# Optimization experiments

Measured on AMD Instinct MI355X. Metric: run time of the kernel, lower is better.

The kernel has to match this reference:

```python
import jax, jax.numpy as jnp
import numpy as np

B, N, T, D, H, E = 2, 1024, 8, 128, 4, 8192
DH = D // H
NEG_SLOPE = 0.2  # GATv2Conv default negative_slope


def _ln(x, g, b):
    m = jnp.mean(x, -1, keepdims=True)
    v = jnp.mean((x - m) ** 2, -1, keepdims=True)
    return (x - m) * jax.lax.rsqrt(v + 1e-5) * g + b


def _forward(x, edge_index, gat_wl, gat_wr, gat_att, gat_b, in_w, in_b, out_w, out_b,
             ffn_w1, ffn_b1, ffn_w2, ffn_b2, fus_w, fus_b,
             lns_g, lns_b, lnt1_g, lnt1_b, lnt2_g, lnt2_b, lnf_g, lnf_b):
    # ---- spatial branch: GATv2, vectorized over (B, T) instead of python loops ----
    loops = jnp.arange(N)
    src = jnp.concatenate([edge_index[0], loops])  # j: message source (PyG adds self loops)
    dst = jnp.concatenate([edge_index[1], loops])  # i: aggregation target
    xl = jnp.einsum('bntd,de->bnte', x, gat_wl).reshape(B, N, T, H, D)
    xr = jnp.einsum('bntd,de->bnte', x, gat_wr).reshape(B, N, T, H, D)
    ml = xl[:, src]                                  # [B,Et,T,H,D]
    mr = xr[:, dst]
    e = jax.nn.leaky_relu(ml + mr, NEG_SLOPE)
    logits = jnp.einsum('bethd,hd->beth', e, gat_att)
    logits = jnp.moveaxis(logits, 1, 0)              # [Et,B,T,H]
    mx = jax.ops.segment_max(logits, dst, num_segments=N)
    p = jnp.exp(logits - mx[dst])                    # stable edge softmax per dst node
    ssum = jax.ops.segment_sum(p, dst, num_segments=N)
    alpha = p / ssum[dst]                            # [Et,B,T,H]
    msg = alpha[..., None] * jnp.moveaxis(ml, 1, 0)
    agg = jax.ops.segment_sum(msg, dst, num_segments=N)  # [N,B,T,H,D]
    x_sp = jnp.moveaxis(agg.mean(3), 0, 1) + gat_b   # concat=False -> head mean; [B,N,T,D]
    x_sp = _ln(x_sp, lns_g, lns_b)

    # ---- temporal branch: MHA + FFN, vectorized over all B*N nodes ----
    xt = x.reshape(B * N, T, D)
    qkv = xt @ in_w + in_b
    q, k, v = jnp.split(qkv, 3, axis=-1)
    q = q.reshape(B * N, T, H, DH)
    k = k.reshape(B * N, T, H, DH)
    v = v.reshape(B * N, T, H, DH)
    scores = jnp.einsum('bthd,bshd->bhts', q, k) / np.float32(np.sqrt(DH))
    attn = jax.nn.softmax(scores, -1)
    o = jnp.einsum('bhts,bshd->bthd', attn, v).reshape(B * N, T, D)
    o = o @ out_w + out_b
    x1 = _ln(xt + o, lnt1_g, lnt1_b)
    ffn = jax.nn.gelu(x1 @ ffn_w1 + ffn_b1, approximate=False) @ ffn_w2 + ffn_b2
    x_tp = _ln(x1 + ffn, lnt2_g, lnt2_b).reshape(B, N, T, D)

    # ---- gated fusion with residual ----
    g = jax.nn.sigmoid(jnp.concatenate([x_sp, x_tp], -1) @ fus_w + fus_b)
    return _ln(g * x_sp + (1.0 - g) * x_tp + x, lnf_g, lnf_b)


def setup_inputs() -> dict:
    key = jax.random.key(0)
    ks = jax.random.split(key, 12)
    s = 0.05
    f = jnp.float32
    return {
        'x': jax.random.normal(ks[0], (B, N, T, D), f),
        'edge_index': jax.random.randint(ks[1], (2, E), 0, N),
        'gat_wl': jax.random.normal(ks[2], (D, H * D), f) * s,
        'gat_wr': jax.random.normal(ks[3], (D, H * D), f) * s,
        'gat_att': jax.random.normal(ks[4], (H, D), f) * s,
        'gat_b': jnp.zeros((D,), f),
        'in_w': jax.random.normal(ks[5], (D, 3 * D), f) * s,
        'in_b': jnp.zeros((3 * D,), f),
        'out_w': jax.random.normal(ks[6], (D, D), f) * s,
        'out_b': jnp.zeros((D,), f),
        'ffn_w1': jax.random.normal(ks[7], (D, 4 * D), f) * s,
        'ffn_b1': jnp.zeros((4 * D,), f),
        'ffn_w2': jax.random.normal(ks[8], (4 * D, D), f) * s,
        'ffn_b2': jnp.zeros((D,), f),
        'fus_w': jax.random.normal(ks[9], (2 * D, D), f) * s,
        'fus_b': jnp.zeros((D,), f),
        'lns_g': jnp.ones((D,), f), 'lns_b': jnp.zeros((D,), f),
        'lnt1_g': jnp.ones((D,), f), 'lnt1_b': jnp.zeros((D,), f),
        'lnt2_g': jnp.ones((D,), f), 'lnt2_b': jnp.zeros((D,), f),
        'lnf_g': jnp.ones((D,), f), 'lnf_b': jnp.zeros((D,), f),
    }


def reference(x, edge_index, gat_wl, gat_wr, gat_att, gat_b, in_w, in_b, out_w, out_b,
              ffn_w1, ffn_b1, ffn_w2, ffn_b2, fus_w, fus_b,
              lns_g, lns_b, lnt1_g, lnt1_b, lnt2_g, lnt2_b, lnf_g, lnf_b):
    return _forward(x, edge_index, gat_wl, gat_wr, gat_att, gat_b, in_w, in_b, out_w, out_b,
                    ffn_w1, ffn_b1, ffn_w2, ffn_b2, fus_w, fus_b,
                    lns_g, lns_b, lnt1_g, lnt1_b, lnt2_g, lnt2_b, lnf_g, lnf_b)
```

## Files before the change

kernel.cpp:

```cpp
#include <hip/hip_runtime.h>
#include <math.h>

#define B_ 2
#define N_ 1024
#define T_ 8
#define D_ 128
#define H_ 4
#define E_ 8192
#define EN_ 9216
#define M_ 16384

typedef unsigned short u16;
using bf16x8 = __attribute__((ext_vector_type(8))) short;
using f32x4  = __attribute__((ext_vector_type(4))) float;

__device__ __forceinline__ float bf2f(unsigned int u) {
  return __uint_as_float(u << 16);
}
__device__ __forceinline__ u16 f2bf(float f) {
  unsigned int x = __float_as_uint(f);
  x += 0x7fffu + ((x >> 16) & 1u);
  return (u16)(x >> 16);
}
__device__ __forceinline__ void load8f(const u16* p, float* f) {
  uint4 u = *(const uint4*)p;
  f[0]=bf2f(u.x & 0xffffu); f[1]=bf2f(u.x >> 16);
  f[2]=bf2f(u.y & 0xffffu); f[3]=bf2f(u.y >> 16);
  f[4]=bf2f(u.z & 0xffffu); f[5]=bf2f(u.z >> 16);
  f[6]=bf2f(u.w & 0xffffu); f[7]=bf2f(u.w >> 16);
}
__device__ __forceinline__ void unpack8(uint4 u, float* f) {
  f[0]=bf2f(u.x & 0xffffu); f[1]=bf2f(u.x >> 16);
  f[2]=bf2f(u.y & 0xffffu); f[3]=bf2f(u.y >> 16);
  f[4]=bf2f(u.z & 0xffffu); f[5]=bf2f(u.z >> 16);
  f[6]=bf2f(u.w & 0xffffu); f[7]=bf2f(u.w >> 16);
}
__device__ __forceinline__ void gl2lds(const u16* g, u16* l) {
  __builtin_amdgcn_global_load_lds(
      (const __attribute__((address_space(1))) unsigned int*)(const void*)g,
      (__attribute__((address_space(3))) unsigned int*)(void*)l,
      16, 0, 0);
}

__device__ __forceinline__ size_t bt_row(int r) {
  return (size_t)(((r >> 13) << 3) | (r & 7)) * 1024 + ((r >> 3) & 1023);
}

__device__ __forceinline__ u16 conv_w_elem(int idx,
    const float* wl, const float* wr, const float* inw, const float* outw,
    const float* f1, const float* f2, const float* fw) {
  const float* src; int base, K, N;
  if      (idx < 65536)  { src = wl;   base = 0;      K = 128; N = 512; }
  else if (idx < 131072) { src = wr;   base = 65536;  K = 128; N = 512; }
  else if (idx < 180224) { src = inw;  base = 131072; K = 128; N = 384; }
  else if (idx < 196608) { src = outw; base = 180224; K = 128; N = 128; }
  else if (idx < 262144) { src = f1;   base = 196608; K = 128; N = 512; }
  else if (idx < 327680) { src = f2;   base = 262144; K = 512; N = 128; }
  else                   { src = fw;   base = 327680; K = 256; N = 128; }
  int o = idx - base;
  int n = o / K, k = o - n * K;
  return f2bf(src[k * N + n]);
}

__global__ __launch_bounds__(1024) void prep_csr_k(const float* __restrict__ x,
    const float* __restrict__ wl, const float* __restrict__ wr,
    const float* __restrict__ inw, const float* __restrict__ outw,
    const float* __restrict__ f1, const float* __restrict__ f2,
    const float* __restrict__ fw,
    u16* __restrict__ XB, u16* __restrict__ WB,
    const int* __restrict__ ei, int* __restrict__ offs, int* __restrict__ srcs) {
  __shared__ int cnt[N_];
  __shared__ int cur[N_];
  int bi = blockIdx.x;
  int tid = threadIdx.x;
  if (bi < 512) {
    int i = (bi * 1024 + tid) * 4;
    float4 v = *(const float4*)&x[i];
    u16 o[4] = {f2bf(v.x), f2bf(v.y), f2bf(v.z), f2bf(v.w)};
    *(ushort4*)&XB[i] = *(ushort4*)o;
    return;
  }
  if (bi < 600) {
    int base = (bi - 512) * 4096 + tid * 4;
#pragma unroll
    for (int j = 0; j < 4; ++j)
      WB[base + j] = conv_w_elem(base + j, wl, wr, inw, outw, f1, f2, fw);
    return;
  }
  cnt[tid] = 0;
  __syncthreads();
  for (int e = tid; e < EN_; e += 1024) {
    int d = (e < E_) ? ei[E_ + e] : (e - E_);
    atomicAdd(&cnt[d], 1);
  }
  __syncthreads();
  int mine = cnt[tid];
  for (int off = 1; off < 1024; off <<= 1) {
    int tv = (tid >= off) ? cnt[tid - off] : 0;
    __syncthreads();
    cnt[tid] += tv;
    __syncthreads();
  }
  int excl = cnt[tid] - mine;
  offs[tid] = excl;
  if (tid == 1023) offs[N_] = cnt[1023];
  cur[tid] = excl;
  __syncthreads();
  for (int e = tid; e < EN_; e += 1024) {
    int d = (e < E_) ? ei[E_ + e] : (e - E_);
    int s = (e < E_) ? ei[e] : (e - E_);
    int pos = atomicAdd(&cur[d], 1);
    srcs[pos] = s;
  }
}

template<int BM, int ACT, int ROUTE>
__device__ __forceinline__ void gemm_tile(int bx, int by,
    const u16* A, int lda, const u16* WT, int K, const float* bias,
    u16* C, int ldc, u16* R0, u16* R1, u16* R2, const float* b2,
    u16* As, u16* Bs) {
  constexpr int MI = BM / 32;
  int tid = threadIdx.x;
  int lane = tid & 63, wid = tid >> 6;
  int lr = lane & 15, lk = lane >> 4;
  int wm = (wid >> 1) * (BM / 2);
  int wn = (wid & 1) * 64;

  u16* Cb; int ldc_; int col0; const float* bias_; int remap;
  if (ROUTE) {
    if (bx < 4)      { Cb = R0; ldc_ = 512; col0 = bx * 128;       bias_ = nullptr; remap = 1; }
    else if (bx < 8) { Cb = R1; ldc_ = 512; col0 = (bx - 4) * 128; bias_ = nullptr; remap = 1; }
    else             { Cb = R2; ldc_ = 384; col0 = (bx - 8) * 128; bias_ = b2;      remap = 0; }
  } else { Cb = C; ldc_ = ldc; col0 = bx * 128; bias_ = bias; remap = 0; }

  f32x4 acc[MI][4] = {};
  for (int k0 = 0; k0 < K; k0 += 32) {
    __syncthreads();
#pragma unroll
    for (int i = 0; i < BM / 64; ++i) {
      int o = tid * 16 + i * 4096;
      int row = o >> 6;
      int col = (o >> 1) & 31;
      gl2lds(A + (size_t)(by * BM + row) * lda + k0 + col,
             (u16*)((char*)As + wid * 1024 + i * 4096));
    }
#pragma unroll
    for (int i = 0; i < 2; ++i) {
      int o = tid * 16 + i * 4096;
      int nrow = o >> 6;
      int col = (o >> 1) & 31;
      gl2lds(WT + (size_t)(bx * 128 + nrow) * K + k0 + col,
             (u16*)((char*)Bs + wid * 1024 + i * 4096));
    }
    __syncthreads();
    bf16x8 bf[4];
#pragma unroll
    for (int ni = 0; ni < 4; ++ni)
      bf[ni] = *(const bf16x8*)&Bs[(wn + ni * 16 + lr) * 32 + lk * 8];
#pragma unroll
    for (int mi = 0; mi < MI; ++mi) {
      bf16x8 af = *(const bf16x8*)&As[(wm + mi * 16 + lr) * 32 + lk * 8];
#pragma unroll
      for (int ni = 0; ni < 4; ++ni)
        acc[mi][ni] = __builtin_amdgcn_mfma_f32_16x16x32_bf16(af, bf[ni], acc[mi][ni], 0, 0, 0);
    }
  }
  float bc[4];
#pragma unroll
  for (int ni = 0; ni < 4; ++ni)
    bc[ni] = bias_ ? bias_[col0 + wn + ni * 16 + lr] : 0.f;
#pragma unroll
  for (int mi = 0; mi < MI; ++mi) {
#pragma unroll
    for (int r = 0; r < 4; ++r) {
      int row = by * BM + wm + mi * 16 + lk * 4 + r;
      size_t orow = (ROUTE && remap) ? bt_row(row) : (size_t)row;
#pragma unroll
      for (int ni = 0; ni < 4; ++ni) {
        int col = col0 + wn + ni * 16 + lr;
        float v = acc[mi][ni][r] + bc[ni];
        if (ACT) v = 0.5f * v * (1.f + erff(v * 0.70710678118f));
        Cb[orow * ldc_ + col] = f2bf(v);
      }
    }
  }
}

template<int EPI>
__device__ __forceinline__ void ln_epilogue(int by, f32x4 (&acc)[2][4],
    const float* bias, const float* xres, const u16* xcat,
    const float* lng, const float* lnb,
    float* o32, u16* o16, int os16, float* rs, float* rq) {
  int tid = threadIdx.x;
  int lane = tid & 63, wid = tid >> 6;
  int lr = lane & 15, lk = lane >> 4;
  int wm = (wid >> 1) * 32, wn = (wid & 1) * 64;
  float bc[4];
#pragma unroll
  for (int ni = 0; ni < 4; ++ni) bc[ni] = bias[wn + ni * 16 + lr];
#pragma unroll
  for (int mi = 0; mi < 2; ++mi) {
#pragma unroll
    for (int r = 0; r < 4; ++r) {
      int row = by * 64 + wm + mi * 16 + lk * 4 + r;
      float s = 0.f, s2 = 0.f;
#pragma unroll
      for (int ni = 0; ni < 4; ++ni) {
        int col = wn + ni * 16 + lr;
        float v = acc[mi][ni][r] + bc[ni];
        if (EPI == 1 || EPI == 2) {
          v += xres[(size_t)row * 128 + col];
        } else {
          float gg = 1.f / (1.f + __expf(-v));
          float xsp = bf2f(xcat[(size_t)row * 256 + col]);
          float xtp = bf2f(xcat[(size_t)row * 256 + 128 + col]);
          v = gg * xsp + (1.f - gg) * xtp + xres[(size_t)row * 128 + col];
        }
        acc[mi][ni][r] = v;
        s += v; s2 += v * v;
      }
      s += __shfl_xor(s, 1, 64); s2 += __shfl_xor(s2, 1, 64);
      s += __shfl_xor(s, 2, 64); s2 += __shfl_xor(s2, 2, 64);
      s += __shfl_xor(s, 4, 64); s2 += __shfl_xor(s2, 4, 64);
      s += __shfl_xor(s, 8, 64); s2 += __shfl_xor(s2, 8, 64);
      if (lr == 0) {
        int rl = wm + mi * 16 + lk * 4 + r;
        rs[rl * 2 + (wid & 1)] = s;
        rq[rl * 2 + (wid & 1)] = s2;
      }
    }
  }
  __syncthreads();
#pragma unroll
  for (int mi = 0; mi < 2; ++mi) {
#pragma unroll
    for (int r = 0; r < 4; ++r) {
      int rl = wm + mi * 16 + lk * 4 + r;
      int row = by * 64 + rl;
      float tot = rs[rl * 2] + rs[rl * 2 + 1];
      float tq = rq[rl * 2] + rq[rl * 2 + 1];
      float mean = tot * (1.f / 128.f);
      float var = tq * (1.f / 128.f) - mean * mean;
      float rinv = rsqrtf(var + 1e-5f);
#pragma unroll
      for (int ni = 0; ni < 4; ++ni) {
        int col = wn + ni * 16 + lr;
        float o = (acc[mi][ni][r] - mean) * rinv * lng[col] + lnb[col];
        if (EPI != 2) o32[(size_t)row * 128 + col] = o;
        if (EPI != 3) o16[(size_t)row * os16 + col] = f2bf(o);
      }
    }
  }
}

__global__ __launch_bounds__(256) void fusion_k(const u16* __restrict__ A,
    const u16* __restrict__ WT, const float* __restrict__ bias,
    const float* __restrict__ xres, const u16* __restrict__ xcat,
    const float* __restrict__ lng, const float* __restrict__ lnb,
    float* __restrict__ o32) {
  __shared__ u16 As[64 * 32];
  __shared__ u16 Bs[128 * 32];
  __shared__ float rs[128], rq[128];
  int by = blockIdx.x;
  int tid = threadIdx.x;
  int lane = tid & 63, wid = tid >> 6;
  int lr = lane & 15, lk = lane >> 4;
  int wm = (wid >> 1) * 32, wn = (wid & 1) * 64;
  const int K = 256;

  f32x4 acc[2][4] = {};
  for (int k0 = 0; k0 < K; k0 += 32) {
    __syncthreads();
    {
      int o = tid * 16;
      gl2lds(A + (size_t)(by * 64 + (o >> 6)) * K + k0 + ((o >> 1) & 31),
             (u16*)((char*)As + wid * 1024));
    }
#pragma unroll
    for (int i = 0; i < 2; ++i) {
      int o = tid * 16 + i * 4096;
      gl2lds(WT + (size_t)(o >> 6) * K + k0 + ((o >> 1) & 31),
             (u16*)((char*)Bs + wid * 1024 + i * 4096));
    }
    __syncthreads();
    bf16x8 bf[4];
#pragma unroll
    for (int ni = 0; ni < 4; ++ni)
      bf[ni] = *(const bf16x8*)&Bs[(wn + ni * 16 + lr) * 32 + lk * 8];
#pragma unroll
    for (int mi = 0; mi < 2; ++mi) {
      bf16x8 af = *(const bf16x8*)&As[(wm + mi * 16 + lr) * 32 + lk * 8];
#pragma unroll
      for (int ni = 0; ni < 4; ++ni)
        acc[mi][ni] = __builtin_amdgcn_mfma_f32_16x16x32_bf16(af, bf[ni], acc[mi][ni], 0, 0, 0);
    }
  }
  ln_epilogue<3>(by, acc, bias, xres, xcat, lng, lnb, o32, nullptr, 0, rs, rq);
}

__global__ __launch_bounds__(256) void proj_k(const u16* __restrict__ XB,
    const u16* __restrict__ WT1, const float* __restrict__ in_b,
    u16* __restrict__ XL, u16* __restrict__ XR, u16* __restrict__ QKV) {
  __shared__ u16 As[128 * 32];
  __shared__ u16 Bs[128 * 32];
  gemm_tile<128, 0, 1>(blockIdx.x, blockIdx.y, XB, 128, WT1, 128, nullptr,
                       nullptr, 0, XL, XR, QKV, in_b, As, Bs);
}

__global__ __launch_bounds__(256) void gat_k(const u16* __restrict__ XL,
    const u16* __restrict__ XR,
    const int* __restrict__ offs, const int* __restrict__ srcs,
    const float* __restrict__ att, const float* __restrict__ gb,
    const float* __restrict__ lng, const float* __restrict__ lnb,
    u16* __restrict__ XCAT) {
  int bid = blockIdx.x;
  int lane = threadIdx.x & 63;
  int wid = threadIdx.x >> 6;
  int xcd = bid & 7;
  int slot = bid >> 3;
  int p = ((slot >> 8) << 3) | xcd;
  int n = (slot & 255) * 4 + wid;
  int b = p >> 3, t = p & 7;
  int dd = (lane & 15) * 8;
  size_t tokn = (size_t)(b * N_ + n) * 8 + t;
  const u16* XLs = XL + (size_t)p * 1024 * 512;

  float mr[8], av[8];
  load8f(XR + ((size_t)p * 1024 + n) * 512 + lane * 8, mr);
  *(float4*)&av[0] = *(const float4*)(att + lane * 8);
  *(float4*)&av[4] = *(const float4*)(att + lane * 8 + 4);

  int beg = offs[n], end = offs[n + 1];
  float sH = 0.f;
  float acc[8] = {0.f, 0.f, 0.f, 0.f, 0.f, 0.f, 0.f, 0.f};
  int i = beg;
  uint4 r0 = *(const uint4*)(XLs + (size_t)srcs[i] * 512 + lane * 8);
  uint4 r1 = r0;
  if (i + 1 < end)
    r1 = *(const uint4*)(XLs + (size_t)srcs[i + 1] * 512 + lane * 8);
  while (i + 1 < end) {
    uint4 c0 = r0, c1 = r1;
    if (i + 2 < end)
      r0 = *(const uint4*)(XLs + (size_t)srcs[i + 2] * 512 + lane * 8);
    if (i + 3 < end)
      r1 = *(const uint4*)(XLs + (size_t)srcs[i + 3] * 512 + lane * 8);
    float ml0[8], ml1[8];
    unpack8(c0, ml0);
    unpack8(c1, ml1);
    float d0 = 0.f, d1 = 0.f;
#pragma unroll
    for (int j = 0; j < 8; ++j) {
      float m0 = ml0[j] + mr[j];
      m0 = fmaxf(m0, 0.2f * m0);
      d0 += m0 * av[j];
      float m1 = ml1[j] + mr[j];
      m1 = fmaxf(m1, 0.2f * m1);
      d1 += m1 * av[j];
    }
    d0 += __shfl_xor(d0, 1, 64); d1 += __shfl_xor(d1, 1, 64);
    d0 += __shfl_xor(d0, 2, 64); d1 += __shfl_xor(d1, 2, 64);
    d0 += __shfl_xor(d0, 4, 64); d1 += __shfl_xor(d1, 4, 64);
    d0 += __shfl_xor(d0, 8, 64); d1 += __shfl_xor(d1, 8, 64);
    float p0 = __expf(d0), p1 = __expf(d1);
    sH += p0 + p1;
#pragma unroll
    for (int j = 0; j < 8; ++j) acc[j] += p0 * ml0[j] + p1 * ml1[j];
    i += 2;
  }
  if (i < end) {
    float ml0[8];
    unpack8(r0, ml0);
    float d0 = 0.f;
#pragma unroll
    for (int j = 0; j < 8; ++j) {
      float m0 = ml0[j] + mr[j];
      m0 = fmaxf(m0, 0.2f * m0);
      d0 += m0 * av[j];
    }
    d0 += __shfl_xor(d0, 1, 64);
    d0 += __shfl_xor(d0, 2, 64);
    d0 += __shfl_xor(d0, 4, 64);
    d0 += __shfl_xor(d0, 8, 64);
    float p0 = __expf(d0);
    sH += p0;
#pragma unroll
    for (int j = 0; j < 8; ++j) acc[j] += p0 * ml0[j];
  }
  float invS = 1.f / sH;
#pragma unroll
  for (int j = 0; j < 8; ++j) acc[j] *= invS;
#pragma unroll
  for (int j = 0; j < 8; ++j) {
    acc[j] += __shfl_xor(acc[j], 16, 64);
    acc[j] += __shfl_xor(acc[j], 32, 64);
  }
#pragma unroll
  for (int j = 0; j < 8; ++j) acc[j] = acc[j] * 0.25f + gb[dd + j];
  float s = 0.f, s2 = 0.f;
#pragma unroll
  for (int j = 0; j < 8; ++j) { s += acc[j]; s2 += acc[j] * acc[j]; }
#pragma unroll
  for (int m = 1; m < 16; m <<= 1) {
    s += __shfl_xor(s, m, 64);
    s2 += __shfl_xor(s2, m, 64);
  }
  float mean = s * (1.f / 128.f);
  float var = s2 * (1.f / 128.f) - mean * mean;
  float r = rsqrtf(var + 1e-5f);
  if (lane < 16) {
    u16 ob[8];
#pragma unroll
    for (int j = 0; j < 8; ++j)
      ob[j] = f2bf((acc[j] - mean) * r * lng[dd + j] + lnb[dd + j]);
    *(uint4*)&XCAT[tokn * 256 + dd] = *(uint4*)ob;
  }
}

__global__ __launch_bounds__(256) void attn_oproj_k(const u16* __restrict__ QKV,
    const u16* __restrict__ WTO, const float* __restrict__ out_b,
    const float* __restrict__ x,
    const float* __restrict__ lnt1_g, const float* __restrict__ lnt1_b,
    float* __restrict__ X1, u16* __restrict__ X1B) {
  __shared__ u16 As[4 * 64 * 32];
  __shared__ u16 Bs[4 * 128 * 32];
  __shared__ float rs[128], rq[128];
  int by = blockIdx.x;
  int tid = threadIdx.x;
  int lane = tid & 63, wid = tid >> 6;

#pragma unroll
  for (int i = 0; i < 8; ++i) {
    int o = tid * 16 + i * 4096;
    int c = o >> 13;
    int wb = o & 8191;
    int nrow = wb >> 6;
    int kin = (wb & 63) >> 1;
    gl2lds(WTO + (size_t)nrow * 128 + c * 32 + kin,
           (u16*)((char*)Bs + wid * 1024 + i * 4096));
  }

  int t = lane >> 3, sidx = lane & 7, dg = lane & 7;
  for (int it = 0; it < 8; ++it) {
    int task = wid * 8 + it;
    int bnl = task >> 2, h = task & 3;
    int bn = by * 8 + bnl;
    const u16* base = QKV + (size_t)bn * 8 * 384;
    float va[8][4];
#pragma unroll
    for (int s2 = 0; s2 < 8; ++s2) {
      ushort4 vv = *(const ushort4*)(base + s2 * 384 + 256 + h * 32 + dg * 4);
      va[s2][0] = bf2f(vv.x); va[s2][1] = bf2f(vv.y);
      va[s2][2] = bf2f(vv.z); va[s2][3] = bf2f(vv.w);
    }
    const u16* qp = base + t * 384 + h * 32;
    const u16* kp = base + sidx * 384 + 128 + h * 32;
    float sc = 0.f;
#pragma unroll
    for (int d0 = 0; d0 < 32; d0 += 8) {
      float q[8], k[8];
      load8f(qp + d0, q);
      load8f(kp + d0, k);
#pragma unroll
      for (int j = 0; j < 8; ++j) sc += q[j] * k[j];
    }
    sc *= 0.17677669529663687f;
    float m = sc;
    m = fmaxf(m, __shfl_xor(m, 1, 64));
    m = fmaxf(m, __shfl_xor(m, 2, 64));
    m = fmaxf(m, __shfl_xor(m, 4, 64));
    float p = __expf(sc - m);
    float S = p;
    S += __shfl_xor(S, 1, 64);
    S += __shfl_xor(S, 2, 64);
    S += __shfl_xor(S, 4, 64);
    float alpha = p / S;
    int tb = lane & 56;
    float o0 = 0.f, o1 = 0.f, o2 = 0.f, o3 = 0.f;
#pragma unroll
    for (int s2 = 0; s2 < 8; ++s2) {
      float a = __shfl(alpha, tb + s2, 64);
      o0 += a * va[s2][0];
      o1 += a * va[s2][1];
      o2 += a * va[s2][2];
      o3 += a * va[s2][3];
    }
    u16 ov[4] = {f2bf(o0), f2bf(o1), f2bf(o2), f2bf(o3)};
    int row = bnl * 8 + t;
    *(ushort4*)&As[h * 2048 + row * 32 + dg * 4] = *(ushort4*)ov;
  }
  __syncthreads();

  int lr = lane & 15, lk = lane >> 4;
  int wm = (wid >> 1) * 32, wn = (wid & 1) * 64;
  f32x4 acc[2][4] = {};
#pragma unroll
  for (int c = 0; c < 4; ++c) {
    bf16x8 bf[4];
#pragma unroll
    for (int ni = 0; ni < 4; ++ni)
      bf[ni] = *(const bf16x8*)&Bs[c * 4096 + (wn + ni * 16 + lr) * 32 + lk * 8];
#pragma unroll
    for (int mi = 0; mi < 2; ++mi) {
      bf16x8 af = *(const bf16x8*)&As[c * 2048 + (wm + mi * 16 + lr) * 32 + lk * 8];
#pragma unroll
      for (int ni = 0; ni < 4; ++ni)
        acc[mi][ni] = __builtin_amdgcn_mfma_f32_16x16x32_bf16(af, bf[ni], acc[mi][ni], 0, 0, 0);
    }
  }
  ln_epilogue<1>(by, acc, out_b, x, nullptr, lnt1_g, lnt1_b, X1, X1B, 128, rs, rq);
}

__global__ __launch_bounds__(256) void ffn_fused_k(const u16* __restrict__ X1B,
    const u16* __restrict__ WTF1, const u16* __restrict__ WTF2,
    const float* __restrict__ b1, const float* __restrict__ b2,
    const float* __restrict__ X1,
    const float* __restrict__ lng, const float* __restrict__ lnb,
    u16* __restrict__ XCATr) {
  __shared__ u16 As[64 * 128];
  __shared__ u16 B1s[64 * 128];
  __shared__ u16 B2s[128 * 64];
  __shared__ u16 Hc[2 * 64 * 40];
  __shared__ float rs[128], rq[128];
  int by = blockIdx.x;
  int tid = threadIdx.x;
  int lane = tid & 63, wid = tid >> 6;
  int lr = lane & 15, lk = lane >> 4;

#pragma unroll
  for (int kc = 0; kc < 4; ++kc) {
    gl2lds(X1B + (size_t)(by * 64 + (tid >> 2)) * 128 + kc * 32 + (tid & 3) * 8,
           (u16*)((char*)As + kc * 4096 + wid * 1024));
  }
  int wr0 = (wid >> 1) * 32, wc0 = (wid & 1) * 32;
  int wm = (wid >> 1) * 32, wn = (wid & 1) * 64;
  f32x4 acc2[2][4] = {};
  for (int nc = 0; nc < 8; ++nc) {
    __syncthreads();
#pragma unroll
    for (int kc = 0; kc < 4; ++kc) {
      gl2lds(WTF1 + (size_t)(nc * 64 + (tid >> 2)) * 128 + kc * 32 + (tid & 3) * 8,
             (u16*)((char*)B1s + kc * 4096 + wid * 1024));
    }
#pragma unroll
    for (int i = 0; i < 4; ++i) {
      int o = tid * 16 + i * 4096;
      int kc2l = o >> 13;
      int wb = o & 8191;
      int nrow = wb >> 6;
      int kin = (wb & 63) >> 1;
      gl2lds(WTF2 + (size_t)nrow * 512 + nc * 64 + kc2l * 32 + kin,
             (u16*)((char*)B2s + wid * 1024 + i * 4096));
    }
    __syncthreads();
    f32x4 a1[2][2] = {};
#pragma unroll
    for (int kc = 0; kc < 4; ++kc) {
      bf16x8 bf0 = *(const bf16x8*)&B1s[kc * 2048 + (wc0 + lr) * 32 + lk * 8];
      bf16x8 bf1 = *(const bf16x8*)&B1s[kc * 2048 + (wc0 + 16 + lr) * 32 + lk * 8];
#pragma unroll
      for (int mi = 0; mi < 2; ++mi) {
        bf16x8 af = *(const bf16x8*)&As[kc * 2048 + (wr0 + mi * 16 + lr) * 32 + lk * 8];
        a1[mi][0] = __builtin_amdgcn_mfma_f32_16x16x32_bf16(af, bf0, a1[mi][0], 0, 0, 0);
        a1[mi][1] = __builtin_amdgcn_mfma_f32_16x16x32_bf16(af, bf1, a1[mi][1], 0, 0, 0);
      }
    }
#pragma unroll
    for (int mi = 0; mi < 2; ++mi) {
#pragma unroll
      for (int r = 0; r < 4; ++r) {
        int row = wr0 + mi * 16 + lk * 4 + r;
#pragma unroll
        for (int ni = 0; ni < 2; ++ni) {
          int cl = wc0 + ni * 16 + lr;
          float v = a1[mi][ni][r] + b1[nc * 64 + cl];
          v = 0.5f * v * (1.f + erff(v * 0.70710678118f));
          Hc[(cl >> 5) * 2560 + row * 40 + (cl & 31)] = f2bf(v);
        }
      }
    }
    __syncthreads();
#pragma unroll
    for (int kc2l = 0; kc2l < 2; ++kc2l) {
      bf16x8 bf[4];
#pragma unroll
      for (int ni = 0; ni < 4; ++ni)
        bf[ni] = *(const bf16x8*)&B2s[kc2l * 4096 + (wn + ni * 16 + lr) * 32 + lk * 8];
#pragma unroll
      for (int mi = 0; mi < 2; ++mi) {
        bf16x8 af = *(const bf16x8*)&Hc[kc2l * 2560 + (wm + mi * 16 + lr) * 40 + lk * 8];
#pragma unroll
        for (int ni = 0; ni < 4; ++ni)
          acc2[mi][ni] = __builtin_amdgcn_mfma_f32_16x16x32_bf16(af, bf[ni], acc2[mi][ni], 0, 0, 0);
      }
    }
  }
  __syncthreads();
  ln_epilogue<2>(by, acc2, b2, X1, nullptr, lng, lnb, nullptr, XCATr, 256, rs, rq);
}

extern "C" void kernel_launch(void* const* d_in, const int* in_sizes, int n_in,
                              void* d_out, int out_size, void* d_ws, size_t ws_size,
                              hipStream_t stream) {
  const float* x       = (const float*)d_in[0];
  const int*   ei      = (const int*)d_in[1];
  const float* gat_att = (const float*)d_in[4];
  const float* gat_b   = (const float*)d_in[5];
  const float* in_b    = (const float*)d_in[7];
  const float* out_b   = (const float*)d_in[9];
  const float* ffn_b1  = (const float*)d_in[11];
  const float* ffn_b2  = (const float*)d_in[13];
  const float* fus_b   = (const float*)d_in[15];
  const float* lns_g   = (const float*)d_in[16];
  const float* lns_b   = (const float*)d_in[17];
  const float* lnt1_g  = (const float*)d_in[18];
  const float* lnt1_b  = (const float*)d_in[19];
  const float* lnt2_g  = (const float*)d_in[20];
  const float* lnt2_b  = (const float*)d_in[21];
  const float* lnf_g   = (const float*)d_in[22];
  const float* lnf_b   = (const float*)d_in[23];

  char* ws = (char*)d_ws;
  u16*   WB    = (u16*)ws;
  u16*   WTO   = WB + 180224;
  u16*   WTF1  = WB + 196608;
  u16*   WTF2  = WB + 262144;
  u16*   WTFUS = WB + 327680;
  int*   OFFS  = (int*)(ws + 3145728);
  int*   SRCS  = (int*)(ws + 3153920);
  u16*   XB   = (u16*)(ws + 4194304);
  u16*   XL   = (u16*)(ws + 8388608);
  u16*   XR   = (u16*)(ws + 25165824);
  float* X1   = (float*)(ws + 41943040);
  u16*   QKV  = (u16*)(ws + 50331648);
  u16*   X1B  = (u16*)(ws + 62914560);
  u16*   XCAT = (u16*)(ws + 67108864);

  prep_csr_k<<<dim3(601), dim3(1024), 0, stream>>>(x,
      (const float*)d_in[2], (const float*)d_in[3], (const float*)d_in[6],
      (const float*)d_in[8], (const float*)d_in[10], (const float*)d_in[12],
      (const float*)d_in[14], XB, WB, ei, OFFS, SRCS);

  proj_k<<<dim3(11, 128), dim3(256), 0, stream>>>(XB, WB, in_b, XL, XR, QKV);

  gat_k<<<dim3(4096), dim3(256), 0, stream>>>(XL, XR, OFFS, SRCS,
      gat_att, gat_b, lns_g, lns_b, XCAT);

  attn_oproj_k<<<dim3(256), dim3(256), 0, stream>>>(QKV, WTO, out_b, x,
      lnt1_g, lnt1_b, X1, X1B);

  ffn_fused_k<<<dim3(256), dim3(256), 0, stream>>>(X1B, WTF1, WTF2,
      ffn_b1, ffn_b2, X1, lnt2_g, lnt2_b, XCAT + 128);

  fusion_k<<<dim3(256), dim3(256), 0, stream>>>(XCAT, WTFUS, fus_b, x, XCAT,
      lnf_g, lnf_b, (float*)d_out);
}
```

Measured before the change: 220.1 us.

## Fuse attention/out-proj/LN1 with FFN/LN2 into one kernel; single-stage proj GEMM

```diff
diff --git a/kernel.cpp b/kernel.cpp
--- a/kernel.cpp
+++ b/kernel.cpp
@@ -114,197 +114,69 @@
   }
 }
 
-template<int BM, int ACT, int ROUTE>
-__device__ __forceinline__ void gemm_tile(int bx, int by,
-    const u16* A, int lda, const u16* WT, int K, const float* bias,
-    u16* C, int ldc, u16* R0, u16* R1, u16* R2, const float* b2,
-    u16* As, u16* Bs) {
-  constexpr int MI = BM / 32;
+__global__ __launch_bounds__(256) void proj_k(const u16* __restrict__ XB,
+    const u16* __restrict__ WT1, const float* __restrict__ in_b,
+    u16* __restrict__ XL, u16* __restrict__ XR, u16* __restrict__ QKV) {
+  __shared__ u16 As[128 * 128];
+  __shared__ u16 Bs[128 * 128];
+  int bx = blockIdx.x, by = blockIdx.y;
   int tid = threadIdx.x;
   int lane = tid & 63, wid = tid >> 6;
   int lr = lane & 15, lk = lane >> 4;
-  int wm = (wid >> 1) * (BM / 2);
-  int wn = (wid & 1) * 64;
-
-  u16* Cb; int ldc_; int col0; const float* bias_; int remap;
-  if (ROUTE) {
-    if (bx < 4)      { Cb = R0; ldc_ = 512; col0 = bx * 128;       bias_ = nullptr; remap = 1; }
-    else if (bx < 8) { Cb = R1; ldc_ = 512; col0 = (bx - 4) * 128; bias_ = nullptr; remap = 1; }
-    else             { Cb = R2; ldc_ = 384; col0 = (bx - 8) * 128; bias_ = b2;      remap = 0; }
-  } else { Cb = C; ldc_ = ldc; col0 = bx * 128; bias_ = bias; remap = 0; }
-
-  f32x4 acc[MI][4] = {};
-  for (int k0 = 0; k0 < K; k0 += 32) {
-    __syncthreads();
-#pragma unroll
-    for (int i = 0; i < BM / 64; ++i) {
+  int wm = (wid >> 1) * 64, wn = (wid & 1) * 64;
+
+#pragma unroll
+  for (int kc = 0; kc < 4; ++kc) {
+#pragma unroll
+    for (int i = 0; i < 2; ++i) {
       int o = tid * 16 + i * 4096;
       int row = o >> 6;
       int col = (o >> 1) & 31;
-      gl2lds(A + (size_t)(by * BM + row) * lda + k0 + col,
-             (u16*)((char*)As + wid * 1024 + i * 4096));
-    }
-#pragma unroll
-    for (int i = 0; i < 2; ++i) {
-      int o = tid * 16 + i * 4096;
-      int nrow = o >> 6;
-      int col = (o >> 1) & 31;
-      gl2lds(WT + (size_t)(bx * 128 + nrow) * K + k0 + col,
-             (u16*)((char*)Bs + wid * 1024 + i * 4096));
-    }
-    __syncthreads();
+      gl2lds(XB + (size_t)(by * 128 + row) * 128 + kc * 32 + col,
+             (u16*)((char*)As + kc * 8192 + i * 4096 + wid * 1024));
+      gl2lds(WT1 + (size_t)(bx * 128 + row) * 128 + kc * 32 + col,
+             (u16*)((char*)Bs + kc * 8192 + i * 4096 + wid * 1024));
+    }
+  }
+  __syncthreads();
+
+  f32x4 acc[4][4] = {};
+#pragma unroll
+  for (int kc = 0; kc < 4; ++kc) {
     bf16x8 bf[4];
 #pragma unroll
     for (int ni = 0; ni < 4; ++ni)
-      bf[ni] = *(const bf16x8*)&Bs[(wn + ni * 16 + lr) * 32 + lk * 8];
-#pragma unroll
-    for (int mi = 0; mi < MI; ++mi) {
-      bf16x8 af = *(const bf16x8*)&As[(wm + mi * 16 + lr) * 32 + lk * 8];
+      bf[ni] = *(const bf16x8*)&Bs[kc * 4096 + (wn + ni * 16 + lr) * 32 + lk * 8];
+#pragma unroll
+    for (int mi = 0; mi < 4; ++mi) {
+      bf16x8 af = *(const bf16x8*)&As[kc * 4096 + (wm + mi * 16 + lr) * 32 + lk * 8];
 #pragma unroll
       for (int ni = 0; ni < 4; ++ni)
         acc[mi][ni] = __builtin_amdgcn_mfma_f32_16x16x32_bf16(af, bf[ni], acc[mi][ni], 0, 0, 0);
     }
   }
+
+  u16* Cb; int ldc_; int col0; const float* bias_; int remap;
+  if (bx < 4)      { Cb = XL;  ldc_ = 512; col0 = bx * 128;       bias_ = nullptr; remap = 1; }
+  else if (bx < 8) { Cb = XR;  ldc_ = 512; col0 = (bx - 4) * 128; bias_ = nullptr; remap = 1; }
+  else             { Cb = QKV; ldc_ = 384; col0 = (bx - 8) * 128; bias_ = in_b;    remap = 0; }
   float bc[4];
 #pragma unroll
   for (int ni = 0; ni < 4; ++ni)
     bc[ni] = bias_ ? bias_[col0 + wn + ni * 16 + lr] : 0.f;
 #pragma unroll
-  for (int mi = 0; mi < MI; ++mi) {
+  for (int mi = 0; mi < 4; ++mi) {
 #pragma unroll
     for (int r = 0; r < 4; ++r) {
-      int row = by * BM + wm + mi * 16 + lk * 4 + r;
-      size_t orow = (ROUTE && remap) ? bt_row(row) : (size_t)row;
+      int row = by * 128 + wm + mi * 16 + lk * 4 + r;
+      size_t orow = remap ? bt_row(row) : (size_t)row;
 #pragma unroll
       for (int ni = 0; ni < 4; ++ni) {
         int col = col0 + wn + ni * 16 + lr;
-        float v = acc[mi][ni][r] + bc[ni];
-        if (ACT) v = 0.5f * v * (1.f + erff(v * 0.70710678118f));
-        Cb[orow * ldc_ + col] = f2bf(v);
-      }
-    }
-  }
-}
-
-template<int EPI>
-__device__ __forceinline__ void ln_epilogue(int by, f32x4 (&acc)[2][4],
-    const float* bias, const float* xres, const u16* xcat,
-    const float* lng, const float* lnb,
-    float* o32, u16* o16, int os16, float* rs, float* rq) {
-  int tid = threadIdx.x;
-  int lane = tid & 63, wid = tid >> 6;
-  int lr = lane & 15, lk = lane >> 4;
-  int wm = (wid >> 1) * 32, wn = (wid & 1) * 64;
-  float bc[4];
-#pragma unroll
-  for (int ni = 0; ni < 4; ++ni) bc[ni] = bias[wn + ni * 16 + lr];
-#pragma unroll
-  for (int mi = 0; mi < 2; ++mi) {
-#pragma unroll
-    for (int r = 0; r < 4; ++r) {
-      int row = by * 64 + wm + mi * 16 + lk * 4 + r;
-      float s = 0.f, s2 = 0.f;
-#pragma unroll
-      for (int ni = 0; ni < 4; ++ni) {
-        int col = wn + ni * 16 + lr;
-        float v = acc[mi][ni][r] + bc[ni];
-        if (EPI == 1 || EPI == 2) {
-          v += xres[(size_t)row * 128 + col];
-        } else {
-          float gg = 1.f / (1.f + __expf(-v));
-          float xsp = bf2f(xcat[(size_t)row * 256 + col]);
-          float xtp = bf2f(xcat[(size_t)row * 256 + 128 + col]);
-          v = gg * xsp + (1.f - gg) * xtp + xres[(size_t)row * 128 + col];
-        }
-        acc[mi][ni][r] = v;
-        s += v; s2 += v * v;
-      }
-      s += __shfl_xor(s, 1, 64); s2 += __shfl_xor(s2, 1, 64);
-      s += __shfl_xor(s, 2, 64); s2 += __shfl_xor(s2, 2, 64);
-      s += __shfl_xor(s, 4, 64); s2 += __shfl_xor(s2, 4, 64);
-      s += __shfl_xor(s, 8, 64); s2 += __shfl_xor(s2, 8, 64);
-      if (lr == 0) {
-        int rl = wm + mi * 16 + lk * 4 + r;
-        rs[rl * 2 + (wid & 1)] = s;
-        rq[rl * 2 + (wid & 1)] = s2;
-      }
-    }
-  }
-  __syncthreads();
-#pragma unroll
-  for (int mi = 0; mi < 2; ++mi) {
-#pragma unroll
-    for (int r = 0; r < 4; ++r) {
-      int rl = wm + mi * 16 + lk * 4 + r;
-      int row = by * 64 + rl;
-      float tot = rs[rl * 2] + rs[rl * 2 + 1];
-      float tq = rq[rl * 2] + rq[rl * 2 + 1];
-      float mean = tot * (1.f / 128.f);
-      float var = tq * (1.f / 128.f) - mean * mean;
-      float rinv = rsqrtf(var + 1e-5f);
-#pragma unroll
-      for (int ni = 0; ni < 4; ++ni) {
-        int col = wn + ni * 16 + lr;
-        float o = (acc[mi][ni][r] - mean) * rinv * lng[col] + lnb[col];
-        if (EPI != 2) o32[(size_t)row * 128 + col] = o;
-        if (EPI != 3) o16[(size_t)row * os16 + col] = f2bf(o);
-      }
-    }
-  }
-}
-
-__global__ __launch_bounds__(256) void fusion_k(const u16* __restrict__ A,
-    const u16* __restrict__ WT, const float* __restrict__ bias,
-    const float* __restrict__ xres, const u16* __restrict__ xcat,
-    const float* __restrict__ lng, const float* __restrict__ lnb,
-    float* __restrict__ o32) {
-  __shared__ u16 As[64 * 32];
-  __shared__ u16 Bs[128 * 32];
-  __shared__ float rs[128], rq[128];
-  int by = blockIdx.x;
-  int tid = threadIdx.x;
-  int lane = tid & 63, wid = tid >> 6;
-  int lr = lane & 15, lk = lane >> 4;
-  int wm = (wid >> 1) * 32, wn = (wid & 1) * 64;
-  const int K = 256;
-
-  f32x4 acc[2][4] = {};
-  for (int k0 = 0; k0 < K; k0 += 32) {
-    __syncthreads();
-    {
-      int o = tid * 16;
-      gl2lds(A + (size_t)(by * 64 + (o >> 6)) * K + k0 + ((o >> 1) & 31),
-             (u16*)((char*)As + wid * 1024));
-    }
-#pragma unroll
-    for (int i = 0; i < 2; ++i) {
-      int o = tid * 16 + i * 4096;
-      gl2lds(WT + (size_t)(o >> 6) * K + k0 + ((o >> 1) & 31),
-             (u16*)((char*)Bs + wid * 1024 + i * 4096));
-    }
-    __syncthreads();
-    bf16x8 bf[4];
-#pragma unroll
-    for (int ni = 0; ni < 4; ++ni)
-      bf[ni] = *(const bf16x8*)&Bs[(wn + ni * 16 + lr) * 32 + lk * 8];
-#pragma unroll
-    for (int mi = 0; mi < 2; ++mi) {
-      bf16x8 af = *(const bf16x8*)&As[(wm + mi * 16 + lr) * 32 + lk * 8];
-#pragma unroll
-      for (int ni = 0; ni < 4; ++ni)
-        acc[mi][ni] = __builtin_amdgcn_mfma_f32_16x16x32_bf16(af, bf[ni], acc[mi][ni], 0, 0, 0);
-    }
-  }
-  ln_epilogue<3>(by, acc, bias, xres, xcat, lng, lnb, o32, nullptr, 0, rs, rq);
-}
-
-__global__ __launch_bounds__(256) void proj_k(const u16* __restrict__ XB,
-    const u16* __restrict__ WT1, const float* __restrict__ in_b,
-    u16* __restrict__ XL, u16* __restrict__ XR, u16* __restrict__ QKV) {
-  __shared__ u16 As[128 * 32];
-  __shared__ u16 Bs[128 * 32];
-  gemm_tile<128, 0, 1>(blockIdx.x, blockIdx.y, XB, 128, WT1, 128, nullptr,
-                       nullptr, 0, XL, XR, QKV, in_b, As, Bs);
+        Cb[orow * ldc_ + col] = f2bf(acc[mi][ni][r] + bc[ni]);
+      }
+    }
+  }
 }
 
 __global__ __launch_bounds__(256) void gat_k(const u16* __restrict__ XL,
@@ -416,17 +288,23 @@
   }
 }
 
-__global__ __launch_bounds__(256) void attn_oproj_k(const u16* __restrict__ QKV,
+__global__ __launch_bounds__(256) void tower_k(const u16* __restrict__ QKV,
     const u16* __restrict__ WTO, const float* __restrict__ out_b,
     const float* __restrict__ x,
     const float* __restrict__ lnt1_g, const float* __restrict__ lnt1_b,
-    float* __restrict__ X1, u16* __restrict__ X1B) {
-  __shared__ u16 As[4 * 64 * 32];
-  __shared__ u16 Bs[4 * 128 * 32];
+    const u16* __restrict__ WTF1, const u16* __restrict__ WTF2,
+    const float* __restrict__ b1, const float* __restrict__ b2,
+    const float* __restrict__ lnt2_g, const float* __restrict__ lnt2_b,
+    u16* __restrict__ XCATr) {
+  __shared__ u16 P[4 * 64 * 32];
+  __shared__ u16 Wb[16384];
+  __shared__ u16 Hc[2 * 64 * 40];
   __shared__ float rs[128], rq[128];
   int by = blockIdx.x;
   int tid = threadIdx.x;
   int lane = tid & 63, wid = tid >> 6;
+  int lr = lane & 15, lk = lane >> 4;
+  int wm = (wid >> 1) * 32, wn = (wid & 1) * 64;
 
 #pragma unroll
   for (int i = 0; i < 8; ++i) {
@@ -436,9 +314,8 @@
     int nrow = wb >> 6;
     int kin = (wb & 63) >> 1;
     gl2lds(WTO + (size_t)nrow * 128 + c * 32 + kin,
-           (u16*)((char*)Bs + wid * 1024 + i * 4096));
-  }
-
+           (u16*)((char*)Wb + wid * 1024 + i * 4096));
+  }
   int t = lane >> 3, sidx = lane & 7, dg = lane & 7;
   for (int it = 0; it < 8; ++it) {
     int task = wid * 8 + it;
@@ -486,60 +363,85 @@
     }
     u16 ov[4] = {f2bf(o0), f2bf(o1), f2bf(o2), f2bf(o3)};
     int row = bnl * 8 + t;
-    *(ushort4*)&As[h * 2048 + row * 32 + dg * 4] = *(ushort4*)ov;
+    *(ushort4*)&P[h * 2048 + row * 32 + dg * 4] = *(ushort4*)ov;
   }
   __syncthreads();
 
-  int lr = lane & 15, lk = lane >> 4;
-  int wm = (wid >> 1) * 32, wn = (wid & 1) * 64;
   f32x4 acc[2][4] = {};
 #pragma unroll
   for (int c = 0; c < 4; ++c) {
     bf16x8 bf[4];
 #pragma unroll
     for (int ni = 0; ni < 4; ++ni)
-      bf[ni] = *(const bf16x8*)&Bs[c * 4096 + (wn + ni * 16 + lr) * 32 + lk * 8];
+      bf[ni] = *(const bf16x8*)&Wb[c * 4096 + (wn + ni * 16 + lr) * 32 + lk * 8];
 #pragma unroll
     for (int mi = 0; mi < 2; ++mi) {
-      bf16x8 af = *(const bf16x8*)&As[c * 2048 + (wm + mi * 16 + lr) * 32 + lk * 8];
+      bf16x8 af = *(const bf16x8*)&P[c * 2048 + (wm + mi * 16 + lr) * 32 + lk * 8];
 #pragma unroll
       for (int ni = 0; ni < 4; ++ni)
         acc[mi][ni] = __builtin_amdgcn_mfma_f32_16x16x32_bf16(af, bf[ni], acc[mi][ni], 0, 0, 0);
     }
   }
-  ln_epilogue<1>(by, acc, out_b, x, nullptr, lnt1_g, lnt1_b, X1, X1B, 128, rs, rq);
-}
-
-__global__ __launch_bounds__(256) void ffn_fused_k(const u16* __restrict__ X1B,
-    const u16* __restrict__ WTF1, const u16* __restrict__ WTF2,
-    const float* __restrict__ b1, const float* __restrict__ b2,
-    const float* __restrict__ X1,
-    const float* __restrict__ lng, const float* __restrict__ lnb,
-    u16* __restrict__ XCATr) {
-  __shared__ u16 As[64 * 128];
-  __shared__ u16 B1s[64 * 128];
-  __shared__ u16 B2s[128 * 64];
-  __shared__ u16 Hc[2 * 64 * 40];
-  __shared__ float rs[128], rq[128];
-  int by = blockIdx.x;
-  int tid = threadIdx.x;
-  int lane = tid & 63, wid = tid >> 6;
-  int lr = lane & 15, lk = lane >> 4;
-
-#pragma unroll
-  for (int kc = 0; kc < 4; ++kc) {
-    gl2lds(X1B + (size_t)(by * 64 + (tid >> 2)) * 128 + kc * 32 + (tid & 3) * 8,
-           (u16*)((char*)As + kc * 4096 + wid * 1024));
-  }
+
+  f32x4 x1r[2][4];
+  {
+    float bc[4];
+#pragma unroll
+    for (int ni = 0; ni < 4; ++ni) bc[ni] = out_b[wn + ni * 16 + lr];
+#pragma unroll
+    for (int mi = 0; mi < 2; ++mi) {
+#pragma unroll
+      for (int r = 0; r < 4; ++r) {
+        int rowl = wm + mi * 16 + lk * 4 + r;
+        int row = by * 64 + rowl;
+        float s = 0.f, s2 = 0.f;
+#pragma unroll
+        for (int ni = 0; ni < 4; ++ni) {
+          int col = wn + ni * 16 + lr;
+          float v = acc[mi][ni][r] + bc[ni] + x[(size_t)row * 128 + col];
+          acc[mi][ni][r] = v;
+          s += v; s2 += v * v;
+        }
+        s += __shfl_xor(s, 1, 64); s2 += __shfl_xor(s2, 1, 64);
+        s += __shfl_xor(s, 2, 64); s2 += __shfl_xor(s2, 2, 64);
+        s += __shfl_xor(s, 4, 64); s2 += __shfl_xor(s2, 4, 64);
+        s += __shfl_xor(s, 8, 64); s2 += __shfl_xor(s2, 8, 64);
+        if (lr == 0) {
+          rs[rowl * 2 + (wid & 1)] = s;
+          rq[rowl * 2 + (wid & 1)] = s2;
+        }
+      }
+    }
+    __syncthreads();
+#pragma unroll
+    for (int mi = 0; mi < 2; ++mi) {
+#pragma unroll
+      for (int r = 0; r < 4; ++r) {
+        int rowl = wm + mi * 16 + lk * 4 + r;
+        float tot = rs[rowl * 2] + rs[rowl * 2 + 1];
+        float tq = rq[rowl * 2] + rq[rowl * 2 + 1];
+        float mean = tot * (1.f / 128.f);
+        float var = tq * (1.f / 128.f) - mean * mean;
+        float rinv = rsqrtf(var + 1e-5f);
+#pragma unroll
+        for (int ni = 0; ni < 4; ++ni) {
+          int col = wn + ni * 16 + lr;
+          float o = (acc[mi][ni][r] - mean) * rinv * lnt1_g[col] + lnt1_b[col];
+          x1r[mi][ni][r] = o;
+          P[(col >> 5) * 2048 + rowl * 32 + (col & 31)] = f2bf(o);
+        }
+      }
+    }
+  }
+
   int wr0 = (wid >> 1) * 32, wc0 = (wid & 1) * 32;
-  int wm = (wid >> 1) * 32, wn = (wid & 1) * 64;
   f32x4 acc2[2][4] = {};
   for (int nc = 0; nc < 8; ++nc) {
     __syncthreads();
 #pragma unroll
     for (int kc = 0; kc < 4; ++kc) {
       gl2lds(WTF1 + (size_t)(nc * 64 + (tid >> 2)) * 128 + kc * 32 + (tid & 3) * 8,
-             (u16*)((char*)B1s + kc * 4096 + wid * 1024));
+             (u16*)((char*)Wb + kc * 4096 + wid * 1024));
     }
 #pragma unroll
     for (int i = 0; i < 4; ++i) {
@@ -549,17 +451,17 @@
       int nrow = wb >> 6;
       int kin = (wb & 63) >> 1;
       gl2lds(WTF2 + (size_t)nrow * 512 + nc * 64 + kc2l * 32 + kin,
-             (u16*)((char*)B2s + wid * 1024 + i * 4096));
+             (u16*)((char*)Wb + 16384 + wid * 1024 + i * 4096));
     }
     __syncthreads();
     f32x4 a1[2][2] = {};
 #pragma unroll
     for (int kc = 0; kc < 4; ++kc) {
-      bf16x8 bf0 = *(const bf16x8*)&B1s[kc * 2048 + (wc0 + lr) * 32 + lk * 8];
-      bf16x8 bf1 = *(const bf16x8*)&B1s[kc * 2048 + (wc0 + 16 + lr) * 32 + lk * 8];
+      bf16x8 bf0 = *(const bf16x8*)&Wb[kc * 2048 + (wc0 + lr) * 32 + lk * 8];
+      bf16x8 bf1 = *(const bf16x8*)&Wb[kc * 2048 + (wc0 + 16 + lr) * 32 + lk * 8];
 #pragma unroll
       for (int mi = 0; mi < 2; ++mi) {
-        bf16x8 af = *(const bf16x8*)&As[kc * 2048 + (wr0 + mi * 16 + lr) * 32 + lk * 8];
+        bf16x8 af = *(const bf16x8*)&P[kc * 2048 + (wr0 + mi * 16 + lr) * 32 + lk * 8];
         a1[mi][0] = __builtin_amdgcn_mfma_f32_16x16x32_bf16(af, bf0, a1[mi][0], 0, 0, 0);
         a1[mi][1] = __builtin_amdgcn_mfma_f32_16x16x32_bf16(af, bf1, a1[mi][1], 0, 0, 0);
       }
@@ -584,7 +486,7 @@
       bf16x8 bf[4];
 #pragma unroll
       for (int ni = 0; ni < 4; ++ni)
-        bf[ni] = *(const bf16x8*)&B2s[kc2l * 4096 + (wn + ni * 16 + lr) * 32 + lk * 8];
+        bf[ni] = *(const bf16x8*)&Wb[8192 + kc2l * 4096 + (wn + ni * 16 + lr) * 32 + lk * 8];
 #pragma unroll
       for (int mi = 0; mi < 2; ++mi) {
         bf16x8 af = *(const bf16x8*)&Hc[kc2l * 2560 + (wm + mi * 16 + lr) * 40 + lk * 8];
@@ -595,7 +497,149 @@
     }
   }
   __syncthreads();
-  ln_epilogue<2>(by, acc2, b2, X1, nullptr, lng, lnb, nullptr, XCATr, 256, rs, rq);
+
+  {
+    float bc[4];
+#pragma unroll
+    for (int ni = 0; ni < 4; ++ni) bc[ni] = b2[wn + ni * 16 + lr];
+#pragma unroll
+    for (int mi = 0; mi < 2; ++mi) {
+#pragma unroll
+      for (int r = 0; r < 4; ++r) {
+        int rowl = wm + mi * 16 + lk * 4 + r;
+        float s = 0.f, s2 = 0.f;
+#pragma unroll
+        for (int ni = 0; ni < 4; ++ni) {
+          float v = acc2[mi][ni][r] + bc[ni] + x1r[mi][ni][r];
+          acc2[mi][ni][r] = v;
+          s += v; s2 += v * v;
+        }
+        s += __shfl_xor(s, 1, 64); s2 += __shfl_xor(s2, 1, 64);
+        s += __shfl_xor(s, 2, 64); s2 += __shfl_xor(s2, 2, 64);
+        s += __shfl_xor(s, 4, 64); s2 += __shfl_xor(s2, 4, 64);
+        s += __shfl_xor(s, 8, 64); s2 += __shfl_xor(s2, 8, 64);
+        if (lr == 0) {
+          rs[rowl * 2 + (wid & 1)] = s;
+          rq[rowl * 2 + (wid & 1)] = s2;
+        }
+      }
+    }
+    __syncthreads();
+#pragma unroll
+    for (int mi = 0; mi < 2; ++mi) {
+#pragma unroll
+      for (int r = 0; r < 4; ++r) {
+        int rowl = wm + mi * 16 + lk * 4 + r;
+        int row = by * 64 + rowl;
+        float tot = rs[rowl * 2] + rs[rowl * 2 + 1];
+        float tq = rq[rowl * 2] + rq[rowl * 2 + 1];
+        float mean = tot * (1.f / 128.f);
+        float var = tq * (1.f / 128.f) - mean * mean;
+        float rinv = rsqrtf(var + 1e-5f);
+#pragma unroll
+        for (int ni = 0; ni < 4; ++ni) {
+          int col = wn + ni * 16 + lr;
+          float o = (acc2[mi][ni][r] - mean) * rinv * lnt2_g[col] + lnt2_b[col];
+          XCATr[(size_t)row * 256 + col] = f2bf(o);
+        }
+      }
+    }
+  }
+}
+
+__global__ __launch_bounds__(256) void fusion_k(const u16* __restrict__ A,
+    const u16* __restrict__ WT, const float* __restrict__ bias,
+    const float* __restrict__ xres, const u16* __restrict__ xcat,
+    const float* __restrict__ lng, const float* __restrict__ lnb,
+    float* __restrict__ o32) {
+  __shared__ u16 As[64 * 32];
+  __shared__ u16 Bs[128 * 32];
+  __shared__ float rs[128], rq[128];
+  int by = blockIdx.x;
+  int tid = threadIdx.x;
+  int lane = tid & 63, wid = tid >> 6;
+  int lr = lane & 15, lk = lane >> 4;
+  int wm = (wid >> 1) * 32, wn = (wid & 1) * 64;
+  const int K = 256;
+
+  f32x4 acc[2][4] = {};
+  for (int k0 = 0; k0 < K; k0 += 32) {
+    __syncthreads();
+    {
+      int o = tid * 16;
+      gl2lds(A + (size_t)(by * 64 + (o >> 6)) * K + k0 + ((o >> 1) & 31),
+             (u16*)((char*)As + wid * 1024));
+    }
+#pragma unroll
+    for (int i = 0; i < 2; ++i) {
+      int o = tid * 16 + i * 4096;
+      gl2lds(WT + (size_t)(o >> 6) * K + k0 + ((o >> 1) & 31),
+             (u16*)((char*)Bs + wid * 1024 + i * 4096));
+    }
+    __syncthreads();
+    bf16x8 bf[4];
+#pragma unroll
+    for (int ni = 0; ni < 4; ++ni)
+      bf[ni] = *(const bf16x8*)&Bs[(wn + ni * 16 + lr) * 32 + lk * 8];
+#pragma unroll
+    for (int mi = 0; mi < 2; ++mi) {
+      bf16x8 af = *(const bf16x8*)&As[(wm + mi * 16 + lr) * 32 + lk * 8];
+#pragma unroll
+      for (int ni = 0; ni < 4; ++ni)
+        acc[mi][ni] = __builtin_amdgcn_mfma_f32_16x16x32_bf16(af, bf[ni], acc[mi][ni], 0, 0, 0);
+    }
+  }
+  float bc[4];
+#pragma unroll
+  for (int ni = 0; ni < 4; ++ni) bc[ni] = bias[wn + ni * 16 + lr];
+#pragma unroll
+  for (int mi = 0; mi < 2; ++mi) {
+#pragma unroll
+    for (int r = 0; r < 4; ++r) {
+      int rowl = wm + mi * 16 + lk * 4 + r;
+      int row = by * 64 + rowl;
+      float s = 0.f, s2 = 0.f;
+#pragma unroll
+      for (int ni = 0; ni < 4; ++ni) {
+        int col = wn + ni * 16 + lr;
+        float v = acc[mi][ni][r] + bc[ni];
+        float gg = 1.f / (1.f + __expf(-v));
+        float xsp = bf2f(xcat[(size_t)row * 256 + col]);
+        float xtp = bf2f(xcat[(size_t)row * 256 + 128 + col]);
+        v = gg * xsp + (1.f - gg) * xtp + xres[(size_t)row * 128 + col];
+        acc[mi][ni][r] = v;
+        s += v; s2 += v * v;
+      }
+      s += __shfl_xor(s, 1, 64); s2 += __shfl_xor(s2, 1, 64);
+      s += __shfl_xor(s, 2, 64); s2 += __shfl_xor(s2, 2, 64);
+      s += __shfl_xor(s, 4, 64); s2 += __shfl_xor(s2, 4, 64);
+      s += __shfl_xor(s, 8, 64); s2 += __shfl_xor(s2, 8, 64);
+      if (lr == 0) {
+        rs[rowl * 2 + (wid & 1)] = s;
+        rq[rowl * 2 + (wid & 1)] = s2;
+      }
+    }
+  }
+  __syncthreads();
+#pragma unroll
+  for (int mi = 0; mi < 2; ++mi) {
+#pragma unroll
+    for (int r = 0; r < 4; ++r) {
+      int rowl = wm + mi * 16 + lk * 4 + r;
+      int row = by * 64 + rowl;
+      float tot = rs[rowl * 2] + rs[rowl * 2 + 1];
+      float tq = rq[rowl * 2] + rq[rowl * 2 + 1];
+      float mean = tot * (1.f / 128.f);
+      float var = tq * (1.f / 128.f) - mean * mean;
+      float rinv = rsqrtf(var + 1e-5f);
+#pragma unroll
+      for (int ni = 0; ni < 4; ++ni) {
+        int col = wn + ni * 16 + lr;
+        o32[(size_t)row * 128 + col] =
+            (acc[mi][ni][r] - mean) * rinv * lng[col] + lnb[col];
+      }
+    }
+  }
 }
 
 extern "C" void kernel_launch(void* const* d_in, const int* in_sizes, int n_in,
@@ -630,9 +674,7 @@
   u16*   XB   = (u16*)(ws + 4194304);
   u16*   XL   = (u16*)(ws + 8388608);
   u16*   XR   = (u16*)(ws + 25165824);
-  float* X1   = (float*)(ws + 41943040);
   u16*   QKV  = (u16*)(ws + 50331648);
-  u16*   X1B  = (u16*)(ws + 62914560);
   u16*   XCAT = (u16*)(ws + 67108864);
 
   prep_csr_k<<<dim3(601), dim3(1024), 0, stream>>>(x,
@@ -645,11 +687,8 @@
   gat_k<<<dim3(4096), dim3(256), 0, stream>>>(XL, XR, OFFS, SRCS,
       gat_att, gat_b, lns_g, lns_b, XCAT);
 
-  attn_oproj_k<<<dim3(256), dim3(256), 0, stream>>>(QKV, WTO, out_b, x,
-      lnt1_g, lnt1_b, X1, X1B);
-
-  ffn_fused_k<<<dim3(256), dim3(256), 0, stream>>>(X1B, WTF1, WTF2,
-      ffn_b1, ffn_b2, X1, lnt2_g, lnt2_b, XCAT + 128);
+  tower_k<<<dim3(256), dim3(256), 0, stream>>>(QKV, WTO, out_b, x,
+      lnt1_g, lnt1_b, WTF1, WTF2, ffn_b1, ffn_b2, lnt2_g, lnt2_b, XCAT + 128);
 
   fusion_k<<<dim3(256), dim3(256), 0, stream>>>(XCAT, WTFUS, fus_b, x, XCAT,
       lnf_g, lnf_b, (float*)d_out);
```

Measured after the change: 215.6 us. -2.1%, faster.
